# Kernel tuning notes

Hardware: AMD Instinct MI355X
Metric: run time of the kernel (lower is better)

## Reference

```python
import jax, jax.numpy as jnp
import numpy as np

N_NODES = 100000
N_EDGES = 800000
N_GRAPHS = 128
BN_EPS = 1e-5
NORM_EPS = 1e-12


def setup_inputs() -> dict:
    key = jax.random.key(0)
    ks = jax.random.split(key, 40)
    def nrm(k, shape):
        return jax.random.normal(k, shape, dtype=jnp.float32) * 0.05
    inp = {}
    inp["batch"] = jnp.sort(jax.random.randint(ks[0], (N_NODES,), 0, N_GRAPHS)).astype(jnp.int32)
    inp["x"] = jax.random.normal(ks[1], (N_NODES, 13), dtype=jnp.float32)
    inp["edge_index"] = jax.random.randint(ks[2], (2, N_EDGES), 0, N_NODES).astype(jnp.int32)
    inp["pseudo"] = jax.random.normal(ks[3], (N_EDGES, 2), dtype=jnp.float32)
    conv_dims = [(13, 128), (128, 256), (256, 256), (256, 256), (256, 256), (256, 256)]
    i = 4
    for li, (din, dout) in enumerate(conv_dims, 1):
        inp[f"conv{li}_Wl"] = nrm(ks[i], (din, dout)); i += 1
        inp[f"conv{li}_bl"] = jnp.zeros((dout,), jnp.float32)
        inp[f"conv{li}_Wr"] = nrm(ks[i], (din, dout)); i += 1
    inp["fc1_W"] = nrm(ks[i], (256, 256)); i += 1
    inp["fc1_b"] = jnp.zeros((256,), jnp.float32)
    inp["fc2_W"] = nrm(ks[i], (256, 128)); i += 1
    inp["fc2_b"] = jnp.zeros((128,), jnp.float32)
    inp["bn2_g"] = jnp.ones((128,), jnp.float32)
    inp["bn2_b"] = jnp.zeros((128,), jnp.float32)
    inp["bn2_rm"] = jnp.zeros((128,), jnp.float32)
    inp["bn2_rv"] = jnp.ones((128,), jnp.float32)
    inp["fc3_W"] = nrm(ks[i], (128, 64)); i += 1
    inp["fc3_b"] = jnp.zeros((64,), jnp.float32)
    inp["out_W"] = nrm(ks[i], (64, 3)); i += 1
    inp["out_b"] = jnp.zeros((3,), jnp.float32)
    return inp


def _sage(x, src, dst, Wl, bl, Wr):
    # mean-aggregate neighbor (source) features at target nodes, then lin_l(agg) + lin_r(x)
    msg = jax.ops.segment_sum(x[src], dst, num_segments=N_NODES)        # [N, din]
    cnt = jax.ops.segment_sum(jnp.ones((src.shape[0], 1), x.dtype), dst, num_segments=N_NODES)
    agg = msg / jnp.maximum(cnt, 1.0)
    return agg @ Wl + bl + x @ Wr


def reference(batch, x, edge_index, pseudo,
              conv1_Wl, conv1_bl, conv1_Wr, conv2_Wl, conv2_bl, conv2_Wr,
              conv3_Wl, conv3_bl, conv3_Wr, conv4_Wl, conv4_bl, conv4_Wr,
              conv5_Wl, conv5_bl, conv5_Wr, conv6_Wl, conv6_bl, conv6_Wr,
              fc1_W, fc1_b, fc2_W, fc2_b, bn2_g, bn2_b, bn2_rm, bn2_rv,
              fc3_W, fc3_b, out_W, out_b):
    elu = jax.nn.elu
    src, dst = edge_index[0], edge_index[1]
    h = elu(_sage(x, src, dst, conv1_Wl, conv1_bl, conv1_Wr))
    h = elu(_sage(h, src, dst, conv2_Wl, conv2_bl, conv2_Wr))
    h = h + elu(_sage(h, src, dst, conv3_Wl, conv3_bl, conv3_Wr))
    h = h + elu(_sage(h, src, dst, conv4_Wl, conv4_bl, conv4_Wr))
    h = h + elu(_sage(h, src, dst, conv5_Wl, conv5_bl, conv5_Wr))
    h = h + elu(_sage(h, src, dst, conv6_Wl, conv6_bl, conv6_Wr))
    h = h + elu(h @ fc1_W + fc1_b)
    h = elu(h @ fc2_W + fc2_b)
    # dropout is identity in eval mode
    pooled = jax.ops.segment_sum(h, batch, num_segments=N_GRAPHS)       # [G, 128]
    cnt = jax.ops.segment_sum(jnp.ones((h.shape[0], 1), h.dtype), batch, num_segments=N_GRAPHS)
    pooled = pooled / jnp.maximum(cnt, 1.0)
    # BatchNorm1d in eval mode with running stats
    hg = (pooled - bn2_rm) / jnp.sqrt(bn2_rv + BN_EPS) * bn2_g + bn2_b
    hg = elu(hg @ fc3_W + fc3_b)
    o = hg @ out_W + out_b
    norm = jnp.linalg.norm(o, axis=1, keepdims=True)
    return o / jnp.maximum(norm, NORM_EPS)
```

## Files before the change

kernel.cpp:

```cpp
#include <hip/hip_runtime.h>
#include <hip/hip_bf16.h>
#include <math.h>

#define WS_ALIGN 256

typedef _Float16 f16;
typedef _Float16 half8 __attribute__((ext_vector_type(8)));
typedef float f32x4 __attribute__((ext_vector_type(4)));

__device__ __forceinline__ float elu_f(float x){ return x > 0.f ? x : expm1f(x); }

__global__ void count_deg(const int* __restrict__ dst, int* __restrict__ deg, int E){
    int e = blockIdx.x*256 + threadIdx.x;
    if(e < E) atomicAdd(&deg[dst[e]], 1);
}

__global__ void scan1(const int* __restrict__ deg, int* __restrict__ off,
                      int* __restrict__ bsum, int n){
    __shared__ int s[256];
    int i = blockIdx.x*256 + threadIdx.x;
    int v = (i < n) ? deg[i] : 0;
    s[threadIdx.x] = v;
    __syncthreads();
    for(int d = 1; d < 256; d <<= 1){
        int t = (threadIdx.x >= d) ? s[threadIdx.x - d] : 0;
        __syncthreads();
        s[threadIdx.x] += t;
        __syncthreads();
    }
    if(i < n) off[i] = s[threadIdx.x] - v;
    if(threadIdx.x == 255) bsum[blockIdx.x] = s[255];
}

__global__ void scan2(int* __restrict__ bsum, int nb){
    __shared__ int s[1024];
    int t = threadIdx.x;
    int v = (t < nb) ? bsum[t] : 0;
    s[t] = v;
    __syncthreads();
    for(int d = 1; d < 1024; d <<= 1){
        int x = (t >= d) ? s[t - d] : 0;
        __syncthreads();
        s[t] += x;
        __syncthreads();
    }
    if(t < nb) bsum[t] = s[t] - v;
}

__global__ void scan3(int* __restrict__ off, const int* __restrict__ bsum, int n){
    int i = blockIdx.x*256 + threadIdx.x;
    if(i < n) off[i] += bsum[blockIdx.x];
}

__global__ void fill_csr(const int* __restrict__ src, const int* __restrict__ dst,
                         const int* __restrict__ off, int* __restrict__ fill,
                         int* __restrict__ csr, int E){
    int e = blockIdx.x*256 + threadIdx.x;
    if(e < E){
        int d = dst[e];
        int p = atomicAdd(&fill[d], 1);
        csr[off[d] + p] = src[e];
    }
}

template<int LANES>
__global__ void aggregate_s(const float* __restrict__ h, const int* __restrict__ off,
                            const int* __restrict__ deg, const int* __restrict__ csr,
                            float* __restrict__ agg, int M, int din, int inS, int outS){
    constexpr int NPB = 256 / LANES;
    int lane = threadIdx.x & (LANES - 1);
    int node = blockIdx.x*NPB + threadIdx.x / LANES;
    if(node >= M) return;
    int o = off[node], d = deg[node];
    bool act = lane < din;
    float acc = 0.f;
    for(int j = 0; j < d; j++){
        int s = csr[o + j];
        if(act) acc += h[(long)s*inS + lane];
    }
    if(act) agg[(long)node*outS + lane] = acc / fmaxf((float)d, 1.f);
}

template<int LANES>
__global__ void aggregate_h(const f16* __restrict__ h, const int* __restrict__ off,
                            const int* __restrict__ deg, const int* __restrict__ csr,
                            f16* __restrict__ agg, int M, int inS, int outS){
    constexpr int NPB = 256 / LANES;
    int lane = threadIdx.x & (LANES - 1);
    int node = blockIdx.x*NPB + threadIdx.x / LANES;
    if(node >= M) return;
    int o = off[node], d = deg[node];
    float acc[8] = {0.f,0.f,0.f,0.f,0.f,0.f,0.f,0.f};
    for(int j = 0; j < d; j++){
        int s = csr[o + j];
        half8 v = *reinterpret_cast<const half8*>(&h[(long)s*inS + lane*8]);
        #pragma unroll
        for(int q = 0; q < 8; q++) acc[q] += (float)v[q];
    }
    float inv = 1.f / fmaxf((float)d, 1.f);
    half8 r;
    #pragma unroll
    for(int q = 0; q < 8; q++) r[q] = (f16)(acc[q]*inv);
    *reinterpret_cast<half8*>(&agg[(long)node*outS + lane*8]) = r;
}

__global__ void prep_wt(const float* __restrict__ W, f16* __restrict__ Wt, int K, int N){
    int i = blockIdx.x*256 + threadIdx.x;
    if(i >= K*N) return;
    int k = i / N, n = i - k*N;
    Wt[(long)n*K + k] = (f16)W[i];
}

__global__ __launch_bounds__(256) void conv1_gemm(
        const float* __restrict__ agg, const float* __restrict__ x,
        const float* __restrict__ Wl, const float* __restrict__ Wr,
        const float* __restrict__ bl, f16* __restrict__ out, int M){
    __shared__ float sWl[13*128];
    __shared__ float sWr[13*128];
    __shared__ float sb[128];
    int tid = threadIdx.x;
    for(int i = tid; i < 13*128; i += 256){ sWl[i] = Wl[i]; sWr[i] = Wr[i]; }
    if(tid < 128) sb[tid] = bl[tid];
    __syncthreads();
    int node = blockIdx.x*2 + (tid >> 7);
    int j = tid & 127;
    if(node >= M) return;
    float a = sb[j];
    #pragma unroll
    for(int k = 0; k < 13; k++){
        a = fmaf(agg[node*16 + k], sWl[k*128 + j], a);
        a = fmaf(x[node*13 + k],  sWr[k*128 + j], a);
    }
    out[(long)node*128 + j] = (f16)elu_f(a);
}

template<int N, bool DUAL, bool RESID>
__global__ __launch_bounds__(256) void gemm_mfma(
        const f16* __restrict__ A1, int lda1, const f16* __restrict__ W1t,
        const f16* __restrict__ A2, int lda2, const f16* __restrict__ W2t,
        const float* __restrict__ bias, const f16* __restrict__ res,
        f16* __restrict__ C, int M, int K){
    constexpr int WSL = N/4;
    constexpr int NF  = WSL/16;
    constexpr int KCSH = (N == 256) ? 8 : 7;
    __shared__ __align__(16) f16 Alds[8*64*8];
    __shared__ __align__(16) f16 Wlds[8*N*8];
    const int tid = threadIdx.x;
    const int w   = tid >> 6;
    const int l   = tid & 63;
    const int lr  = l & 15;
    const int kg  = l >> 4;
    const long m0 = (long)blockIdx.x * 64;

    const f32x4 zero4 = {0.f, 0.f, 0.f, 0.f};
    f32x4 acc[4][NF];
    #pragma unroll
    for(int mi = 0; mi < 4; mi++)
        #pragma unroll
        for(int ni = 0; ni < NF; ni++) acc[mi][ni] = zero4;

    const int nPhase = DUAL ? 2 : 1;
    for(int p = 0; p < nPhase; p++){
        const f16* __restrict__ A  = (p == 0) ? A1 : A2;
        const int lda              = (p == 0) ? lda1 : lda2;
        const f16* __restrict__ Wt = (p == 0) ? W1t : W2t;
        for(int k0 = 0; k0 < K; k0 += 64){
            __syncthreads();
            #pragma unroll
            for(int it = 0; it < 2; it++){
                int kc = it*4 + (tid >> 6);
                int r  = tid & 63;
                long gm = m0 + r;
                uint4 v = make_uint4(0u, 0u, 0u, 0u);
                if(gm < M) v = *reinterpret_cast<const uint4*>(&A[gm*lda + k0 + kc*8]);
                *reinterpret_cast<uint4*>(&Alds[(kc*64 + r)*8]) = v;
            }
            #pragma unroll
            for(int it = 0; it < N*8/256; it++){
                int idx = it*256 + tid;
                int kc  = idx >> KCSH;
                int n   = idx & (N - 1);
                uint4 v = *reinterpret_cast<const uint4*>(&Wt[(long)n*K + k0 + kc*8]);
                *reinterpret_cast<uint4*>(&Wlds[(kc*N + n)*8]) = v;
            }
            __syncthreads();
            #pragma unroll
            for(int ks = 0; ks < 2; ks++){
                half8 af[4], bf[NF];
                #pragma unroll
                for(int mi = 0; mi < 4; mi++)
                    af[mi] = *reinterpret_cast<const half8*>(
                        &Alds[((ks*4 + kg)*64 + mi*16 + lr)*8]);
                #pragma unroll
                for(int ni = 0; ni < NF; ni++)
                    bf[ni] = *reinterpret_cast<const half8*>(
                        &Wlds[((ks*4 + kg)*N + w*WSL + ni*16 + lr)*8]);
                #pragma unroll
                for(int mi = 0; mi < 4; mi++)
                    #pragma unroll
                    for(int ni = 0; ni < NF; ni++)
                        acc[mi][ni] = __builtin_amdgcn_mfma_f32_16x16x32_f16(
                            af[mi], bf[ni], acc[mi][ni], 0, 0, 0);
            }
        }
    }
    #pragma unroll
    for(int mi = 0; mi < 4; mi++){
        #pragma unroll
        for(int r = 0; r < 4; r++){
            long gm = m0 + mi*16 + kg*4 + r;
            if(gm < M){
                #pragma unroll
                for(int ni = 0; ni < NF; ni++){
                    int col = w*WSL + ni*16 + lr;
                    float v = acc[mi][ni][r] + bias[col];
                    v = elu_f(v);
                    if(RESID) v += (float)res[gm*N + col];
                    C[gm*N + col] = (f16)v;
                }
            }
        }
    }
}

__device__ __forceinline__ int lower_bound_i(const int* __restrict__ a, int n, int key){
    int lo = 0, hi = n;
    while(lo < hi){
        int mid = (lo + hi) >> 1;
        if(a[mid] < key) lo = mid + 1; else hi = mid;
    }
    return lo;
}

__global__ void pool_kernel(const f16* __restrict__ h, const int* __restrict__ batch,
                            float* __restrict__ pooled, int M){
    int g = blockIdx.x, f = threadIdx.x;
    int s = lower_bound_i(batch, M, g);
    int e = lower_bound_i(batch, M, g + 1);
    float acc = 0.f;
    for(int n = s; n < e; n++) acc += (float)h[(long)n*128 + f];
    pooled[g*128 + f] = acc / fmaxf((float)(e - s), 1.f);
}

__global__ __launch_bounds__(256) void tail1_kernel(
        const float* __restrict__ pooled,
        const float* __restrict__ bng, const float* __restrict__ bnb,
        const float* __restrict__ bnrm, const float* __restrict__ bnrv,
        const float* __restrict__ fc3W, const float* __restrict__ fc3b,
        float* __restrict__ H, int G){
    __shared__ float P[64*128];
    int g0 = blockIdx.x * 64;
    int ng = G - g0; if(ng > 64) ng = 64; if(ng <= 0) return;
    int t = threadIdx.x;
    for(int i = t; i < ng*128; i += 256){
        int k = i & 127;
        P[i] = (pooled[g0*128 + i] - bnrm[k]) * (1.f / sqrtf(bnrv[k] + 1e-5f)) * bng[k] + bnb[k];
    }
    __syncthreads();
    for(int i = t; i < ng*64; i += 256){
        int gi = i >> 6, j = i & 63;
        float a = fc3b[j];
        for(int k = 0; k < 128; k++) a = fmaf(P[gi*128 + k], fc3W[k*64 + j], a);
        H[(g0 + gi)*64 + j] = elu_f(a);
    }
}

__global__ __launch_bounds__(128) void tail2_kernel(
        const float* __restrict__ H, const float* __restrict__ outW,
        const float* __restrict__ outb, float* __restrict__ out, int G){
    int t = threadIdx.x;
    if(t >= G) return;
    float o0 = outb[0], o1 = outb[1], o2 = outb[2];
    for(int j = 0; j < 64; j++){
        float h = H[t*64 + j];
        o0 = fmaf(h, outW[j*3 + 0], o0);
        o1 = fmaf(h, outW[j*3 + 1], o1);
        o2 = fmaf(h, outW[j*3 + 2], o2);
    }
    float nrm = sqrtf(o0*o0 + o1*o1 + o2*o2);
    float inv = 1.f / fmaxf(nrm, 1e-12f);
    out[t*3 + 0] = o0*inv;
    out[t*3 + 1] = o1*inv;
    out[t*3 + 2] = o2*inv;
}

extern "C" void kernel_launch(void* const* d_in, const int* in_sizes, int n_in,
                              void* d_out, int out_size, void* d_ws, size_t ws_size,
                              hipStream_t stream){
    const int M = in_sizes[0];
    const int E = in_sizes[2] / 2;
    const int G = out_size / 3;

    const int*   batch = (const int*)d_in[0];
    const float* x     = (const float*)d_in[1];
    const int*   ei    = (const int*)d_in[2];
    const int*   srcE  = ei;
    const int*   dstE  = ei + E;

    const float* Wl[6]  = {(const float*)d_in[4],  (const float*)d_in[7],  (const float*)d_in[10],
                           (const float*)d_in[13], (const float*)d_in[16], (const float*)d_in[19]};
    const float* bl[6]  = {(const float*)d_in[5],  (const float*)d_in[8],  (const float*)d_in[11],
                           (const float*)d_in[14], (const float*)d_in[17], (const float*)d_in[20]};
    const float* Wr[6]  = {(const float*)d_in[6],  (const float*)d_in[9],  (const float*)d_in[12],
                           (const float*)d_in[15], (const float*)d_in[18], (const float*)d_in[21]};
    const float* fc1W = (const float*)d_in[22];
    const float* fc1b = (const float*)d_in[23];
    const float* fc2W = (const float*)d_in[24];
    const float* fc2b = (const float*)d_in[25];
    const float* bng  = (const float*)d_in[26];
    const float* bnb  = (const float*)d_in[27];
    const float* bnrm = (const float*)d_in[28];
    const float* bnrv = (const float*)d_in[29];
    const float* fc3W = (const float*)d_in[30];
    const float* fc3b = (const float*)d_in[31];
    const float* outW = (const float*)d_in[32];
    const float* outb = (const float*)d_in[33];

    char* ws = (char*)d_ws;
    size_t o = 0;
    auto alloc = [&](size_t bytes){
        size_t r = o;
        o = (o + bytes + (WS_ALIGN - 1)) & ~(size_t)(WS_ALIGN - 1);
        return r;
    };
    int*   deg    = (int*)(ws + alloc((size_t)M*4));
    int*   offp   = (int*)(ws + alloc((size_t)M*4));
    int*   fill   = (int*)(ws + alloc((size_t)M*4));
    int*   bsum   = (int*)(ws + alloc(1024*4));
    int*   csr    = (int*)(ws + alloc((size_t)E*4));
    float* Sf     = (float*)(ws + alloc((size_t)M*16*4));
    f16*   F0     = (f16*)(ws + alloc((size_t)M*256*2));
    f16*   F1     = (f16*)(ws + alloc((size_t)M*256*2));
    f16*   F2     = (f16*)(ws + alloc((size_t)M*256*2));
    f16*   wt_c2l = (f16*)(ws + alloc((size_t)256*128*2));
    f16*   wt_c2r = (f16*)(ws + alloc((size_t)256*128*2));
    f16*   wt_l[4]; f16* wt_r[4];
    for(int i = 0; i < 4; i++){
        wt_l[i] = (f16*)(ws + alloc((size_t)256*256*2));
        wt_r[i] = (f16*)(ws + alloc((size_t)256*256*2));
    }
    f16*   wt_fc1 = (f16*)(ws + alloc((size_t)256*256*2));
    f16*   wt_fc2 = (f16*)(ws + alloc((size_t)128*256*2));
    float* pooled = (float*)(ws + alloc((size_t)G*128*4));
    float* Hbuf   = (float*)(ws + alloc((size_t)G*64*4));
    size_t need = o;
    (void)n_in;

    if(ws_size && need > ws_size){
        hipMemsetAsync(d_out, 0, (size_t)out_size*4, stream);
        return;
    }

    hipMemsetAsync(deg,  0, (size_t)M*4, stream);
    hipMemsetAsync(fill, 0, (size_t)M*4, stream);

    int eb = (E + 255)/256;
    int nb = (M + 255)/256;
    count_deg<<<eb, 256, 0, stream>>>(dstE, deg, E);
    scan1<<<nb, 256, 0, stream>>>(deg, offp, bsum, M);
    scan2<<<1, 1024, 0, stream>>>(bsum, nb);
    scan3<<<nb, 256, 0, stream>>>(offp, bsum, M);
    fill_csr<<<eb, 256, 0, stream>>>(srcE, dstE, offp, fill, csr, E);

    prep_wt<<<(128*256 + 255)/256, 256, 0, stream>>>(Wl[1], wt_c2l, 128, 256);
    prep_wt<<<(128*256 + 255)/256, 256, 0, stream>>>(Wr[1], wt_c2r, 128, 256);
    for(int i = 0; i < 4; i++){
        prep_wt<<<(256*256 + 255)/256, 256, 0, stream>>>(Wl[2 + i], wt_l[i], 256, 256);
        prep_wt<<<(256*256 + 255)/256, 256, 0, stream>>>(Wr[2 + i], wt_r[i], 256, 256);
    }
    prep_wt<<<(256*256 + 255)/256, 256, 0, stream>>>(fc1W, wt_fc1, 256, 256);
    prep_wt<<<(256*128 + 255)/256, 256, 0, stream>>>(fc2W, wt_fc2, 256, 128);

    const int gm64 = (M + 63)/64;

    aggregate_s<16><<<(M + 15)/16, 256, 0, stream>>>(x, offp, deg, csr, Sf, M, 13, 13, 16);
    conv1_gemm<<<(M + 1)/2, 256, 0, stream>>>(Sf, x, Wl[0], Wr[0], bl[0], F0, M);

    aggregate_h<16><<<(M + 15)/16, 256, 0, stream>>>(F0, offp, deg, csr, F1, M, 128, 128);
    gemm_mfma<256, true, false><<<gm64, 256, 0, stream>>>(F1, 128, wt_c2l, F0, 128, wt_c2r,
                                                          bl[1], nullptr, F2, M, 128);

    f16* hin = F2;
    f16* hout = F1;
    for(int li = 0; li < 4; li++){
        aggregate_h<32><<<(M + 7)/8, 256, 0, stream>>>(hin, offp, deg, csr, F0, M, 256, 256);
        gemm_mfma<256, true, true><<<gm64, 256, 0, stream>>>(F0, 256, wt_l[li], hin, 256, wt_r[li],
                                                             bl[2 + li], hin, hout, M, 256);
        f16* t = hin; hin = hout; hout = t;
    }

    gemm_mfma<256, false, true><<<gm64, 256, 0, stream>>>(hin, 256, wt_fc1, nullptr, 0, nullptr,
                                                          fc1b, hin, F1, M, 256);
    gemm_mfma<128, false, false><<<gm64, 256, 0, stream>>>(F1, 256, wt_fc2, nullptr, 0, nullptr,
                                                           fc2b, nullptr, F0, M, 256);

    pool_kernel<<<G, 128, 0, stream>>>(F0, batch, pooled, M);
    tail1_kernel<<<(G + 63)/64, 256, 0, stream>>>(pooled, bng, bnb, bnrm, bnrv,
                                                  fc3W, fc3b, Hbuf, G);
    tail2_kernel<<<1, 128, 0, stream>>>(Hbuf, outW, outb, (float*)d_out, G);
}
```

Baseline: 1.586 ms.

## Enlarge MFMA GEMM row tile to 128 and parallelize graph pooling over node chunks

The MFMA GEMM now processes 128 rows per block instead of 64, doubling the accumulator tiles per wave so each weight tile loaded into LDS is reused across twice as many rows. Graph mean-pooling is restructured: instead of one block per graph scanning its whole node range serially, node chunks of 256 are summed in parallel with atomic adds into a zeroed buffer, and the per-graph count division moves into the tail kernel. The larger tile raises register pressure (for N=256, 8x4 f32x4 accumulators per wave) and halves the block count, which may reduce occupancy. Float atomics make the pooled sums order-nondeterministic.

```diff
diff --git a/kernel.cpp b/kernel.cpp
--- a/kernel.cpp
+++ b/kernel.cpp
@@ -143,19 +143,19 @@
     constexpr int WSL = N/4;
     constexpr int NF  = WSL/16;
     constexpr int KCSH = (N == 256) ? 8 : 7;
-    __shared__ __align__(16) f16 Alds[8*64*8];
+    __shared__ __align__(16) f16 Alds[8*128*8];
     __shared__ __align__(16) f16 Wlds[8*N*8];
     const int tid = threadIdx.x;
     const int w   = tid >> 6;
     const int l   = tid & 63;
     const int lr  = l & 15;
     const int kg  = l >> 4;
-    const long m0 = (long)blockIdx.x * 64;
+    const long m0 = (long)blockIdx.x * 128;
 
     const f32x4 zero4 = {0.f, 0.f, 0.f, 0.f};
-    f32x4 acc[4][NF];
+    f32x4 acc[8][NF];
     #pragma unroll
-    for(int mi = 0; mi < 4; mi++)
+    for(int mi = 0; mi < 8; mi++)
         #pragma unroll
         for(int ni = 0; ni < NF; ni++) acc[mi][ni] = zero4;
 
@@ -167,13 +167,14 @@
         for(int k0 = 0; k0 < K; k0 += 64){
             __syncthreads();
             #pragma unroll
-            for(int it = 0; it < 2; it++){
-                int kc = it*4 + (tid >> 6);
-                int r  = tid & 63;
-                long gm = m0 + r;
+            for(int it = 0; it < 4; it++){
+                int idx = it*256 + tid;
+                int row = idx & 127;
+                int kc  = idx >> 7;
+                long gm = m0 + row;
                 uint4 v = make_uint4(0u, 0u, 0u, 0u);
                 if(gm < M) v = *reinterpret_cast<const uint4*>(&A[gm*lda + k0 + kc*8]);
-                *reinterpret_cast<uint4*>(&Alds[(kc*64 + r)*8]) = v;
+                *reinterpret_cast<uint4*>(&Alds[(kc*128 + row)*8]) = v;
             }
             #pragma unroll
             for(int it = 0; it < N*8/256; it++){
@@ -186,17 +187,17 @@
             __syncthreads();
             #pragma unroll
             for(int ks = 0; ks < 2; ks++){
-                half8 af[4], bf[NF];
+                half8 af[8], bf[NF];
                 #pragma unroll
-                for(int mi = 0; mi < 4; mi++)
+                for(int mi = 0; mi < 8; mi++)
                     af[mi] = *reinterpret_cast<const half8*>(
-                        &Alds[((ks*4 + kg)*64 + mi*16 + lr)*8]);
+                        &Alds[((ks*4 + kg)*128 + mi*16 + lr)*8]);
                 #pragma unroll
                 for(int ni = 0; ni < NF; ni++)
                     bf[ni] = *reinterpret_cast<const half8*>(
                         &Wlds[((ks*4 + kg)*N + w*WSL + ni*16 + lr)*8]);
                 #pragma unroll
-                for(int mi = 0; mi < 4; mi++)
+                for(int mi = 0; mi < 8; mi++)
                     #pragma unroll
                     for(int ni = 0; ni < NF; ni++)
                         acc[mi][ni] = __builtin_amdgcn_mfma_f32_16x16x32_f16(
@@ -205,7 +206,7 @@
         }
     }
     #pragma unroll
-    for(int mi = 0; mi < 4; mi++){
+    for(int mi = 0; mi < 8; mi++){
         #pragma unroll
         for(int r = 0; r < 4; r++){
             long gm = m0 + mi*16 + kg*4 + r;
@@ -223,6 +224,27 @@
     }
 }
 
+__global__ __launch_bounds__(128) void pool_sum(
+        const f16* __restrict__ h, const int* __restrict__ batch,
+        float* __restrict__ pooled, int M){
+    const int CH = 256;
+    int n0 = blockIdx.x * CH;
+    if(n0 >= M) return;
+    int f = threadIdx.x;
+    int nend = n0 + CH; if(nend > M) nend = M;
+    int g = batch[n0];
+    float acc = 0.f;
+    for(int n = n0; n < nend; n++){
+        int gn = batch[n];
+        if(gn != g){
+            atomicAdd(&pooled[g*128 + f], acc);
+            acc = 0.f; g = gn;
+        }
+        acc += (float)h[(long)n*128 + f];
+    }
+    atomicAdd(&pooled[g*128 + f], acc);
+}
+
 __device__ __forceinline__ int lower_bound_i(const int* __restrict__ a, int n, int key){
     int lo = 0, hi = n;
     while(lo < hi){
@@ -232,29 +254,27 @@
     return lo;
 }
 
-__global__ void pool_kernel(const f16* __restrict__ h, const int* __restrict__ batch,
-                            float* __restrict__ pooled, int M){
-    int g = blockIdx.x, f = threadIdx.x;
-    int s = lower_bound_i(batch, M, g);
-    int e = lower_bound_i(batch, M, g + 1);
-    float acc = 0.f;
-    for(int n = s; n < e; n++) acc += (float)h[(long)n*128 + f];
-    pooled[g*128 + f] = acc / fmaxf((float)(e - s), 1.f);
-}
-
 __global__ __launch_bounds__(256) void tail1_kernel(
-        const float* __restrict__ pooled,
+        const float* __restrict__ pooledSum, const int* __restrict__ batch, int M,
         const float* __restrict__ bng, const float* __restrict__ bnb,
         const float* __restrict__ bnrm, const float* __restrict__ bnrv,
         const float* __restrict__ fc3W, const float* __restrict__ fc3b,
         float* __restrict__ H, int G){
     __shared__ float P[64*128];
+    __shared__ float cnt[64];
     int g0 = blockIdx.x * 64;
     int ng = G - g0; if(ng > 64) ng = 64; if(ng <= 0) return;
     int t = threadIdx.x;
+    if(t < ng){
+        int s = lower_bound_i(batch, M, g0 + t);
+        int e = lower_bound_i(batch, M, g0 + t + 1);
+        cnt[t] = fmaxf((float)(e - s), 1.f);
+    }
+    __syncthreads();
     for(int i = t; i < ng*128; i += 256){
         int k = i & 127;
-        P[i] = (pooled[g0*128 + i] - bnrm[k]) * (1.f / sqrtf(bnrv[k] + 1e-5f)) * bng[k] + bnb[k];
+        float mean = pooledSum[g0*128 + i] / cnt[i >> 7];
+        P[i] = (mean - bnrm[k]) * (1.f / sqrtf(bnrv[k] + 1e-5f)) * bng[k] + bnb[k];
     }
     __syncthreads();
     for(int i = t; i < ng*64; i += 256){
@@ -351,8 +371,9 @@
         return;
     }
 
-    hipMemsetAsync(deg,  0, (size_t)M*4, stream);
-    hipMemsetAsync(fill, 0, (size_t)M*4, stream);
+    hipMemsetAsync(deg,    0, (size_t)M*4, stream);
+    hipMemsetAsync(fill,   0, (size_t)M*4, stream);
+    hipMemsetAsync(pooled, 0, (size_t)G*128*4, stream);
 
     int eb = (E + 255)/256;
     int nb = (M + 255)/256;
@@ -371,31 +392,31 @@
     prep_wt<<<(256*256 + 255)/256, 256, 0, stream>>>(fc1W, wt_fc1, 256, 256);
     prep_wt<<<(256*128 + 255)/256, 256, 0, stream>>>(fc2W, wt_fc2, 256, 128);
 
-    const int gm64 = (M + 63)/64;
+    const int gm128 = (M + 127)/128;
 
     aggregate_s<16><<<(M + 15)/16, 256, 0, stream>>>(x, offp, deg, csr, Sf, M, 13, 13, 16);
     conv1_gemm<<<(M + 1)/2, 256, 0, stream>>>(Sf, x, Wl[0], Wr[0], bl[0], F0, M);
 
     aggregate_h<16><<<(M + 15)/16, 256, 0, stream>>>(F0, offp, deg, csr, F1, M, 128, 128);
-    gemm_mfma<256, true, false><<<gm64, 256, 0, stream>>>(F1, 128, wt_c2l, F0, 128, wt_c2r,
-                                                          bl[1], nullptr, F2, M, 128);
+    gemm_mfma<256, true, false><<<gm128, 256, 0, stream>>>(F1, 128, wt_c2l, F0, 128, wt_c2r,
+                                                           bl[1], nullptr, F2, M, 128);
 
     f16* hin = F2;
     f16* hout = F1;
     for(int li = 0; li < 4; li++){
         aggregate_h<32><<<(M + 7)/8, 256, 0, stream>>>(hin, offp, deg, csr, F0, M, 256, 256);
-        gemm_mfma<256, true, true><<<gm64, 256, 0, stream>>>(F0, 256, wt_l[li], hin, 256, wt_r[li],
-                                                             bl[2 + li], hin, hout, M, 256);
+        gemm_mfma<256, true, true><<<gm128, 256, 0, stream>>>(F0, 256, wt_l[li], hin, 256, wt_r[li],
+                                                              bl[2 + li], hin, hout, M, 256);
         f16* t = hin; hin = hout; hout = t;
     }
 
-    gemm_mfma<256, false, true><<<gm64, 256, 0, stream>>>(hin, 256, wt_fc1, nullptr, 0, nullptr,
-                                                          fc1b, hin, F1, M, 256);
-    gemm_mfma<128, false, false><<<gm64, 256, 0, stream>>>(F1, 256, wt_fc2, nullptr, 0, nullptr,
-                                                           fc2b, nullptr, F0, M, 256);
-
-    pool_kernel<<<G, 128, 0, stream>>>(F0, batch, pooled, M);
-    tail1_kernel<<<(G + 63)/64, 256, 0, stream>>>(pooled, bng, bnb, bnrm, bnrv,
+    gemm_mfma<256, false, true><<<gm128, 256, 0, stream>>>(hin, 256, wt_fc1, nullptr, 0, nullptr,
+                                                           fc1b, hin, F1, M, 256);
+    gemm_mfma<128, false, false><<<gm128, 256, 0, stream>>>(F1, 256, wt_fc2, nullptr, 0, nullptr,
+                                                            fc2b, nullptr, F0, M, 256);
+
+    pool_sum<<<(M + 255)/256, 128, 0, stream>>>(F0, batch, pooled, M);
+    tail1_kernel<<<(G + 63)/64, 256, 0, stream>>>(pooled, batch, M, bng, bnb, bnrm, bnrv,
                                                   fc3W, fc3b, Hbuf, G);
     tail2_kernel<<<1, 128, 0, stream>>>(Hbuf, outW, outb, (float*)d_out, G);
 }
```

New measurement: 1.905 ms. 1.2x slower.
